# Performance work log

Hardware: AMD Instinct MI355X
Metric: run time of the kernel (lower is better)

Reference implementation:

```python
import jax, jax.numpy as jnp
import numpy as np

N, E, D, C, L = 50000, 600000, 128, 40, 4  # nodes, edges, feat dim, classes, conv layers
BN_EPS = 1e-5


def hardswish(x):
    return x * jnp.clip(x + 3.0, 0.0, 6.0) * (1.0 / 6.0)


def setup_inputs() -> dict:
    key = jax.random.key(0)
    ks = jax.random.split(key, 20)
    x = jax.random.normal(ks[0], (N, D), dtype=jnp.float32)
    src = jax.random.randint(ks[1], (E,), 0, N)
    off = jax.random.randint(ks[2], (E,), 1, N)  # guarantees dst != src
    dst = (src + off) % N
    s = 1.0 / np.sqrt(D)
    inp = {
        'x': x, 'src': src, 'dst': dst,
        # per-layer attentional aggregation params (stacked over L layers)
        'Wg': jax.random.normal(ks[3], (L, D, 1), dtype=jnp.float32) * s,
        'bg': jnp.zeros((L, 1), dtype=jnp.float32),
        'Wt': jax.random.normal(ks[4], (L, D, D), dtype=jnp.float32) * s,
        'bt': jnp.zeros((L, D), dtype=jnp.float32),
        # per-layer transform: Linear -> BN(eval) -> Hardswish -> Linear
        'W1': jax.random.normal(ks[5], (L, D, D), dtype=jnp.float32) * s,
        'b1': jnp.zeros((L, D), dtype=jnp.float32),
        'bn_gamma': 0.5 + jax.random.uniform(ks[6], (L, D), dtype=jnp.float32),
        'bn_beta': jax.random.normal(ks[7], (L, D), dtype=jnp.float32) * 0.1,
        'bn_mean': jax.random.normal(ks[8], (L, D), dtype=jnp.float32) * 0.1,
        'bn_var': 0.5 + jax.random.uniform(ks[9], (L, D), dtype=jnp.float32),
        'W2': jax.random.normal(ks[10], (L, D, D), dtype=jnp.float32) * s,
        'b2': jnp.zeros((L, D), dtype=jnp.float32),
        # post_mp head
        'Wp1': jax.random.normal(ks[11], (D, D), dtype=jnp.float32) * s,
        'bp1': jnp.zeros((D,), dtype=jnp.float32),
        'Wp2': jax.random.normal(ks[12], (D, C), dtype=jnp.float32) * s,
        'bp2': jnp.zeros((C,), dtype=jnp.float32),
    }
    return inp


def reference(x, src, dst, Wg, bg, Wt, bt, W1, b1, bn_gamma, bn_beta, bn_mean, bn_var, W2, b2, Wp1, bp1, Wp2, bp2):
    n = x.shape[0]
    loops = jnp.arange(n)
    s = jnp.concatenate([src, loops])  # add_remaining_self_loops
    d = jnp.concatenate([dst, loops])
    h = x
    for i in range(Wg.shape[0]):
        xj = h[s]                                    # gather source feats [E+N, D]
        gate = (xj @ Wg[i] + bg[i])[:, 0]            # attention logit per edge
        m = jax.ops.segment_max(gate, d, num_segments=n)
        e = jnp.exp(gate - m[d])
        denom = jax.ops.segment_sum(e, d, num_segments=n)
        w = e / denom[d]                             # per-dest softmax weight
        hj = xj @ Wt[i] + bt[i]                      # transform_node_feats
        agg = jax.ops.segment_sum(w[:, None] * hj, d, num_segments=n)
        z = agg @ W1[i] + b1[i]
        z = (z - bn_mean[i]) * jax.lax.rsqrt(bn_var[i] + BN_EPS) * bn_gamma[i] + bn_beta[i]
        z = hardswish(z)
        h = z @ W2[i] + b2[i]
        h = hardswish(h)                             # outer F.hardswish in GNN.forward
    h = hardswish(h @ Wp1 + bp1)
    logits = h @ Wp2 + bp2
    return jax.nn.log_softmax(logits, axis=-1)
```

## Files before the change

### kernel.cpp

```cpp
#include <hip/hip_runtime.h>
#include <math.h>

#define FD 128
#define CLS 40
#define BN_EPS 1e-5f
#define AS_STRIDE 136

typedef short short8 __attribute__((ext_vector_type(8)));
typedef float floatx4 __attribute__((ext_vector_type(4)));
typedef unsigned short ushort4v __attribute__((ext_vector_type(4)));
typedef unsigned short u16;
typedef unsigned int u32;

__device__ __forceinline__ u16 bf16_of(float v) {
    unsigned int u = __float_as_uint(v);
    unsigned int r = u + 0x7FFFu + ((u >> 16) & 1u);
    return (u16)(r >> 16);
}
__device__ __forceinline__ float bf16f(u16 h) {
    return __uint_as_float(((unsigned int)h) << 16);
}
__device__ __forceinline__ float blo(u32 v) { return __uint_as_float(v << 16); }
__device__ __forceinline__ float bhi(u32 v) { return __uint_as_float(v & 0xFFFF0000u); }
__device__ __forceinline__ float hswish(float x) {
    return x * fminf(fmaxf(x + 3.0f, 0.0f), 6.0f) * (1.0f / 6.0f);
}

__global__ void hist_kernel(const int* __restrict__ dst, int* __restrict__ cnt,
                            int* __restrict__ rank, int E) {
    int e = blockIdx.x * 256 + threadIdx.x;
    if (e < E) rank[e] = atomicAdd(&cnt[dst[e]], 1);
}

__global__ __launch_bounds__(256) void scan_p1(const int* __restrict__ cnt,
                                               int* __restrict__ bsum, int Nn) {
    const int t = threadIdx.x, b = blockIdx.x;
    int i = b * 256 + t;
    int v = (i < Nn) ? cnt[i] : 0;
    #pragma unroll
    for (int o = 32; o; o >>= 1) v += __shfl_xor(v, o);
    __shared__ int ws[4];
    if ((t & 63) == 0) ws[t >> 6] = v;
    __syncthreads();
    if (t == 0) bsum[b] = ws[0] + ws[1] + ws[2] + ws[3];
}

__global__ __launch_bounds__(256) void scan_p2(int* __restrict__ bsum, int NB,
                                               int* __restrict__ offs, int Nn) {
    __shared__ int wsum[4];
    __shared__ int run_s;
    const int t = threadIdx.x, lane = t & 63, wid = t >> 6;
    if (t == 0) run_s = 0;
    __syncthreads();
    for (int base = 0; base < NB; base += 256) {
        int i = base + t;
        int v = (i < NB) ? bsum[i] : 0;
        int x = v;
        #pragma unroll
        for (int o = 1; o < 64; o <<= 1) {
            int y = __shfl_up(x, o);
            if (lane >= o) x += y;
        }
        if (lane == 63) wsum[wid] = x;
        __syncthreads();
        int pre = run_s;
        #pragma unroll
        for (int w = 0; w < 4; ++w) { if (w < wid) pre += wsum[w]; }
        if (i < NB) bsum[i] = pre + x - v;
        __syncthreads();
        if (t == 0) run_s += wsum[0] + wsum[1] + wsum[2] + wsum[3];
        __syncthreads();
    }
    if (t == 0) offs[Nn] = run_s;
}

__global__ __launch_bounds__(256) void scan_p3(const int* __restrict__ cnt,
                                               const int* __restrict__ bsum,
                                               int* __restrict__ offs, int Nn) {
    __shared__ int wsum[4];
    const int t = threadIdx.x, b = blockIdx.x, lane = t & 63, wid = t >> 6;
    int i = b * 256 + t;
    int v = (i < Nn) ? cnt[i] : 0;
    int x = v;
    #pragma unroll
    for (int o = 1; o < 64; o <<= 1) {
        int y = __shfl_up(x, o);
        if (lane >= o) x += y;
    }
    if (lane == 63) wsum[wid] = x;
    __syncthreads();
    int pre = bsum[b];
    #pragma unroll
    for (int w = 0; w < 4; ++w) { if (w < wid) pre += wsum[w]; }
    if (i < Nn) offs[i] = pre + x - v;
}

__global__ void scatter_kernel(const int* __restrict__ src, const int* __restrict__ dst,
                               const int* __restrict__ offs, const int* __restrict__ rank,
                               int* __restrict__ col, int E) {
    int e = blockIdx.x * 256 + threadIdx.x;
    if (e < E) col[offs[dst[e]] + rank[e]] = src[e];
}

__global__ void prep_weights(const float* __restrict__ Wt, const float* __restrict__ W1,
                             const float* __restrict__ W2, const float* __restrict__ Wp1,
                             const float* __restrict__ Wp2, const float* __restrict__ Wg,
                             u16* __restrict__ wbuf, int L) {
    const int m = blockIdx.y;
    const int id = blockIdx.x * 256 + threadIdx.x;
    const int nsq = 3 * L + 1;
    if (m < nsq) {
        u16* base = wbuf + (size_t)m * 32768;
        const float* src = (m < L) ? Wt + m * 16384
                         : (m < 2 * L) ? W1 + (m - L) * 16384
                         : (m < 3 * L) ? W2 + (m - 2 * L) * 16384
                         : Wp1;
        int n = id >> 7, k = id & 127;
        base[n * 128 + k] = bf16_of(src[k * 128 + n]);
    } else if (m == nsq) {
        if (id >= 48 * 128) return;
        u16* base = wbuf + (size_t)m * 32768;
        int n = id >> 7, k = id & 127;
        base[n * 128 + k] = bf16_of((n < CLS) ? Wp2[k * CLS + n] : 0.f);
    } else {
        int gi = m - (nsq + 1);
        if (id >= 2048) return;
        u16* base = wbuf + (size_t)(nsq + 1) * 32768 + (size_t)gi * 4096;
        base[id] = bf16_of((id < 128) ? Wg[gi * 128 + id] : 0.f);
    }
}

__device__ __forceinline__ void stage_f32(const float* __restrict__ A, int m0, int M,
                                          u16* As, int t) {
    #pragma unroll
    for (int i = 0; i < 8; ++i) {
        int id = i * 256 + t;
        int row = id >> 5, c4 = id & 31;
        float4 v = make_float4(0.f, 0.f, 0.f, 0.f);
        if (m0 + row < M) v = ((const float4*)A)[(size_t)(m0 + row) * 32 + c4];
        ushort4v hh = {bf16_of(v.x), bf16_of(v.y), bf16_of(v.z), bf16_of(v.w)};
        *(ushort4v*)(&As[row * AS_STRIDE + c4 * 4]) = hh;
    }
}

__device__ __forceinline__ void stage_bf16(const u16* __restrict__ A, int m0, int M,
                                           u16* As, int t) {
    #pragma unroll
    for (int i = 0; i < 4; ++i) {
        int id = i * 256 + t;
        int row = id >> 4, c8 = id & 15;
        short8 v = {0, 0, 0, 0, 0, 0, 0, 0};
        if (m0 + row < M) v = ((const short8*)A)[(size_t)(m0 + row) * 16 + c8];
        *(short8*)(&As[row * AS_STRIDE + c8 * 8]) = v;
    }
}

struct Bfrags { short8 h[2][4]; };

__device__ __forceinline__ void load_B(const u16* __restrict__ Bh,
                                       int ct0, int l16, int quad, Bfrags& f) {
    #pragma unroll
    for (int c = 0; c < 2; ++c)
        #pragma unroll
        for (int kc = 0; kc < 4; ++kc) {
            int boff = ((ct0 + c) * 16 + l16) * 128 + kc * 32 + quad * 8;
            f.h[c][kc] = *(const short8*)(&Bh[boff]);
        }
}

__device__ __forceinline__ void gemm_ct2(const u16* As, const Bfrags& f, int l16, int quad,
                                         floatx4 (&acc)[4][2]) {
    #pragma unroll
    for (int kc = 0; kc < 4; ++kc) {
        short8 a[4];
        #pragma unroll
        for (int rt = 0; rt < 4; ++rt)
            a[rt] = *(const short8*)(&As[(rt * 16 + l16) * AS_STRIDE + kc * 32 + quad * 8]);
        #pragma unroll
        for (int rt = 0; rt < 4; ++rt)
            #pragma unroll
            for (int c = 0; c < 2; ++c)
                acc[rt][c] = __builtin_amdgcn_mfma_f32_16x16x32_bf16(a[rt], f.h[c][kc], acc[rt][c], 0, 0, 0);
    }
}

#define ZERO_ACC(acc) { _Pragma("unroll") for (int rt = 0; rt < 4; ++rt) \
    { acc[rt][0] = (floatx4){0.f,0.f,0.f,0.f}; acc[rt][1] = (floatx4){0.f,0.f,0.f,0.f}; } }

__device__ __forceinline__ void gate_panel(const u16* As, const u16* __restrict__ Gh,
                                           const float* __restrict__ bg,
                                           float* __restrict__ gate,
                                           int m0, int M, int l16, int quad) {
    floatx4 gacc[4];
    #pragma unroll
    for (int rt = 0; rt < 4; ++rt) gacc[rt] = (floatx4){0.f, 0.f, 0.f, 0.f};
    #pragma unroll
    for (int kc = 0; kc < 4; ++kc) {
        int boff = l16 * 128 + kc * 32 + quad * 8;
        short8 gh = *(const short8*)(&Gh[boff]);
        #pragma unroll
        for (int rt = 0; rt < 4; ++rt) {
            short8 a = *(const short8*)(&As[(rt * 16 + l16) * AS_STRIDE + kc * 32 + quad * 8]);
            gacc[rt] = __builtin_amdgcn_mfma_f32_16x16x32_bf16(a, gh, gacc[rt], 0, 0, 0);
        }
    }
    if (l16 == 0) {
        float b0 = bg[0];
        #pragma unroll
        for (int rt = 0; rt < 4; ++rt)
            #pragma unroll
            for (int reg = 0; reg < 4; ++reg) {
                int row = m0 + rt * 16 + quad * 4 + reg;
                if (row < M) gate[row] = gacc[rt][reg] + b0;
            }
    }
}

__global__ __launch_bounds__(256, 3) void gemm_gate_kernel(
    const float* __restrict__ Af,
    const u16* __restrict__ Gh, const float* __restrict__ bg,
    const u16* __restrict__ Bh, const float* __restrict__ bt,
    u16* __restrict__ ht, float* __restrict__ gate, int M) {
    __shared__ __align__(16) u16 As[64 * AS_STRIDE];
    const int t = threadIdx.x, m0 = blockIdx.x * 64;
    const int w = t >> 6, lane = t & 63, l16 = lane & 15, quad = lane >> 4, ct0 = w * 2;
    Bfrags f;
    load_B(Bh, ct0, l16, quad, f);
    stage_f32(Af, m0, M, As, t);
    __syncthreads();
    floatx4 acc[4][2];
    ZERO_ACC(acc);
    gemm_ct2(As, f, l16, quad, acc);
    if (w == 0) gate_panel(As, Gh, bg, gate, m0, M, l16, quad);
    #pragma unroll
    for (int c = 0; c < 2; ++c) {
        int cc = (ct0 + c) * 16 + l16;
        float b = bt[cc];
        #pragma unroll
        for (int rt = 0; rt < 4; ++rt)
            #pragma unroll
            for (int reg = 0; reg < 4; ++reg) {
                int row = m0 + rt * 16 + quad * 4 + reg;
                if (row < M) ht[(size_t)row * 128 + cc] = bf16_of(acc[rt][c][reg] + b);
            }
    }
}

__global__ __launch_bounds__(256) void agg_kernel(const float* __restrict__ gate,
                                                  const u32* __restrict__ ht32,
                                                  const int* __restrict__ offs,
                                                  const int* __restrict__ col,
                                                  u32* __restrict__ aggb, int Nn) {
    int gt = blockIdx.x * 256 + threadIdx.x;
    int n = gt >> 6, lane = gt & 63;
    if (n >= Nn) return;
    int beg = offs[n], end = offs[n + 1];
    float gs = gate[n];
    float denom0 = 1.0f, denom1 = 0.f;
    u32 sv = ht32[(size_t)n * 64 + lane];
    float a0 = blo(sv), a1 = bhi(sv);
    float b0 = 0.f, b1 = 0.f;
    int e = beg;
    for (; e + 8 <= end; e += 8) {
        int c[8];
        #pragma unroll
        for (int j = 0; j < 8; ++j) c[j] = col[e + j];
        float g[8];
        #pragma unroll
        for (int j = 0; j < 8; ++j) g[j] = gate[c[j]];
        u32 v[8];
        #pragma unroll
        for (int j = 0; j < 8; ++j) v[j] = ht32[(size_t)c[j] * 64 + lane];
        float wj[8];
        #pragma unroll
        for (int j = 0; j < 8; ++j) wj[j] = __expf(g[j] - gs);
        denom0 += (wj[0] + wj[1]) + (wj[2] + wj[3]);
        denom1 += (wj[4] + wj[5]) + (wj[6] + wj[7]);
        #pragma unroll
        for (int j = 0; j < 4; ++j) {
            a0 += wj[j] * blo(v[j]);
            a1 += wj[j] * bhi(v[j]);
        }
        #pragma unroll
        for (int j = 4; j < 8; ++j) {
            b0 += wj[j] * blo(v[j]);
            b1 += wj[j] * bhi(v[j]);
        }
    }
    for (; e < end; ++e) {
        int c = col[e];
        float w = __expf(gate[c] - gs);
        u32 v = ht32[(size_t)c * 64 + lane];
        denom0 += w;
        a0 += w * blo(v);
        a1 += w * bhi(v);
    }
    float inv = 1.0f / (denom0 + denom1);
    float r0 = (a0 + b0) * inv, r1 = (a1 + b1) * inv;
    aggb[(size_t)n * 64 + lane] = (u32)bf16_of(r0) | ((u32)bf16_of(r1) << 16);
}

__global__ __launch_bounds__(256, 3) void layer_mid_kernel(
    const u16* __restrict__ A,
    const u16* __restrict__ B1h, const float* __restrict__ b1,
    const float* __restrict__ bng, const float* __restrict__ bnb,
    const float* __restrict__ bnm, const float* __restrict__ bnv,
    const u16* __restrict__ B2h, const float* __restrict__ b2,
    const u16* __restrict__ Wth, const float* __restrict__ bt,
    const u16* __restrict__ Gh, const float* __restrict__ bg,
    u16* __restrict__ htb, float* __restrict__ gate, int M) {
    __shared__ __align__(16) u16 As[64 * AS_STRIDE];
    __shared__ __align__(16) u16 Zs[64 * AS_STRIDE];
    const int t = threadIdx.x, m0 = blockIdx.x * 64;
    const int w = t >> 6, lane = t & 63, l16 = lane & 15, quad = lane >> 4, ct0 = w * 2;
    Bfrags f;
    load_B(B1h, ct0, l16, quad, f);
    stage_bf16(A, m0, M, As, t);
    __syncthreads();
    floatx4 acc[4][2];
    ZERO_ACC(acc);
    gemm_ct2(As, f, l16, quad, acc);
    #pragma unroll
    for (int c = 0; c < 2; ++c) {
        int cc = (ct0 + c) * 16 + l16;
        float sc = bng[cc] * rsqrtf(bnv[cc] + BN_EPS);
        float sh = bnb[cc] - bnm[cc] * sc;
        float bb = b1[cc];
        #pragma unroll
        for (int rt = 0; rt < 4; ++rt)
            #pragma unroll
            for (int reg = 0; reg < 4; ++reg) {
                int r = rt * 16 + quad * 4 + reg;
                Zs[r * AS_STRIDE + cc] = bf16_of(hswish((acc[rt][c][reg] + bb) * sc + sh));
            }
    }
    load_B(B2h, ct0, l16, quad, f);
    __syncthreads();
    ZERO_ACC(acc);
    gemm_ct2(Zs, f, l16, quad, acc);
    #pragma unroll
    for (int c = 0; c < 2; ++c) {
        int cc = (ct0 + c) * 16 + l16;
        float b = b2[cc];
        #pragma unroll
        for (int rt = 0; rt < 4; ++rt)
            #pragma unroll
            for (int reg = 0; reg < 4; ++reg) {
                int r = rt * 16 + quad * 4 + reg;
                As[r * AS_STRIDE + cc] = bf16_of(hswish(acc[rt][c][reg] + b));
            }
    }
    load_B(Wth, ct0, l16, quad, f);
    __syncthreads();
    ZERO_ACC(acc);
    gemm_ct2(As, f, l16, quad, acc);
    if (w == 0) gate_panel(As, Gh, bg, gate, m0, M, l16, quad);
    #pragma unroll
    for (int c = 0; c < 2; ++c) {
        int cc = (ct0 + c) * 16 + l16;
        float b = bt[cc];
        #pragma unroll
        for (int rt = 0; rt < 4; ++rt)
            #pragma unroll
            for (int reg = 0; reg < 4; ++reg) {
                int row = m0 + rt * 16 + quad * 4 + reg;
                if (row < M) htb[(size_t)row * 128 + cc] = bf16_of(acc[rt][c][reg] + b);
            }
    }
}

__global__ __launch_bounds__(256, 3) void layer_final_kernel(
    const u16* __restrict__ A,
    const u16* __restrict__ B1h, const float* __restrict__ b1,
    const float* __restrict__ bng, const float* __restrict__ bnb,
    const float* __restrict__ bnm, const float* __restrict__ bnv,
    const u16* __restrict__ B2h, const float* __restrict__ b2,
    const u16* __restrict__ P1h, const float* __restrict__ bp1,
    const u16* __restrict__ P2h, const float* __restrict__ bp2,
    float* __restrict__ out, int M) {
    __shared__ __align__(16) u16 As[64 * AS_STRIDE];
    __shared__ __align__(16) u16 Zs[64 * AS_STRIDE];
    const int t = threadIdx.x, m0 = blockIdx.x * 64;
    const int w = t >> 6, lane = t & 63, l16 = lane & 15, quad = lane >> 4, ct0 = w * 2;
    Bfrags f;
    load_B(B1h, ct0, l16, quad, f);
    stage_bf16(A, m0, M, As, t);
    __syncthreads();
    floatx4 acc[4][2];
    ZERO_ACC(acc);
    gemm_ct2(As, f, l16, quad, acc);
    #pragma unroll
    for (int c = 0; c < 2; ++c) {
        int cc = (ct0 + c) * 16 + l16;
        float sc = bng[cc] * rsqrtf(bnv[cc] + BN_EPS);
        float sh = bnb[cc] - bnm[cc] * sc;
        float bb = b1[cc];
        #pragma unroll
        for (int rt = 0; rt < 4; ++rt)
            #pragma unroll
            for (int reg = 0; reg < 4; ++reg) {
                int r = rt * 16 + quad * 4 + reg;
                Zs[r * AS_STRIDE + cc] = bf16_of(hswish((acc[rt][c][reg] + bb) * sc + sh));
            }
    }
    load_B(B2h, ct0, l16, quad, f);
    __syncthreads();
    ZERO_ACC(acc);
    gemm_ct2(Zs, f, l16, quad, acc);
    #pragma unroll
    for (int c = 0; c < 2; ++c) {
        int cc = (ct0 + c) * 16 + l16;
        float b = b2[cc];
        #pragma unroll
        for (int rt = 0; rt < 4; ++rt)
            #pragma unroll
            for (int reg = 0; reg < 4; ++reg) {
                int r = rt * 16 + quad * 4 + reg;
                As[r * AS_STRIDE + cc] = bf16_of(hswish(acc[rt][c][reg] + b));
            }
    }
    load_B(P1h, ct0, l16, quad, f);
    __syncthreads();
    ZERO_ACC(acc);
    gemm_ct2(As, f, l16, quad, acc);
    #pragma unroll
    for (int c = 0; c < 2; ++c) {
        int cc = (ct0 + c) * 16 + l16;
        float bb = bp1[cc];
        #pragma unroll
        for (int rt = 0; rt < 4; ++rt)
            #pragma unroll
            for (int reg = 0; reg < 4; ++reg) {
                int r = rt * 16 + quad * 4 + reg;
                Zs[r * AS_STRIDE + cc] = bf16_of(hswish(acc[rt][c][reg] + bb));
            }
    }
    __syncthreads();
    const int wr0 = w * 16;
    floatx4 acc2[3];
    #pragma unroll
    for (int ct = 0; ct < 3; ++ct) acc2[ct] = (floatx4){0.f, 0.f, 0.f, 0.f};
    #pragma unroll
    for (int kc = 0; kc < 4; ++kc) {
        short8 a = *(const short8*)(&Zs[(wr0 + l16) * AS_STRIDE + kc * 32 + quad * 8]);
        #pragma unroll
        for (int ct = 0; ct < 3; ++ct) {
            int boff = (ct * 16 + l16) * 128 + kc * 32 + quad * 8;
            short8 bh = *(const short8*)(&P2h[boff]);
            acc2[ct] = __builtin_amdgcn_mfma_f32_16x16x32_bf16(a, bh, acc2[ct], 0, 0, 0);
        }
    }
    #pragma unroll
    for (int reg = 0; reg < 4; ++reg) {
        float v[3];
        #pragma unroll
        for (int ct = 0; ct < 3; ++ct) {
            int c = ct * 16 + l16;
            v[ct] = (c < CLS) ? acc2[ct][reg] + bp2[c] : -INFINITY;
        }
        float mx = fmaxf(fmaxf(v[0], v[1]), v[2]);
        #pragma unroll
        for (int o = 1; o < 16; o <<= 1) mx = fmaxf(mx, __shfl_xor(mx, o));
        float s = 0.f;
        #pragma unroll
        for (int ct = 0; ct < 3; ++ct) s += (v[ct] > -INFINITY) ? __expf(v[ct] - mx) : 0.f;
        #pragma unroll
        for (int o = 1; o < 16; o <<= 1) s += __shfl_xor(s, o);
        float lse = mx + __logf(s);
        int row = m0 + wr0 + quad * 4 + reg;
        if (row < M) {
            #pragma unroll
            for (int ct = 0; ct < 3; ++ct) {
                int c = ct * 16 + l16;
                if (c < CLS) out[(size_t)row * CLS + c] = v[ct] - lse;
            }
        }
    }
}

extern "C" void kernel_launch(void* const* d_in, const int* in_sizes, int n_in,
                              void* d_out, int out_size, void* d_ws, size_t ws_size,
                              hipStream_t stream) {
    const float* x   = (const float*)d_in[0];
    const int*   src = (const int*)d_in[1];
    const int*   dst = (const int*)d_in[2];
    const float* Wg  = (const float*)d_in[3];
    const float* bg  = (const float*)d_in[4];
    const float* Wt  = (const float*)d_in[5];
    const float* bt  = (const float*)d_in[6];
    const float* W1  = (const float*)d_in[7];
    const float* b1  = (const float*)d_in[8];
    const float* bng = (const float*)d_in[9];
    const float* bnb = (const float*)d_in[10];
    const float* bnm = (const float*)d_in[11];
    const float* bnv = (const float*)d_in[12];
    const float* W2  = (const float*)d_in[13];
    const float* b2  = (const float*)d_in[14];
    const float* Wp1 = (const float*)d_in[15];
    const float* bp1 = (const float*)d_in[16];
    const float* Wp2 = (const float*)d_in[17];
    const float* bp2 = (const float*)d_in[18];
    float* out = (float*)d_out;

    const int N = in_sizes[0] / FD;
    const int E = in_sizes[1];
    const int L = in_sizes[3] / FD;
    const int nsq = 3 * L + 1;
    const int NB = (N + 255) / 256;

    u16* htb    = (u16*)d_ws;
    u16* aggb   = htb + (size_t)N * FD;
    float* gate = (float*)(aggb + (size_t)N * FD);
    u16* wbuf   = (u16*)(gate + N);
    size_t wslots = (size_t)(nsq + 1) * 32768 + (size_t)L * 4096;
    int* counts = (int*)(wbuf + wslots);
    int* offs   = counts + N;
    int* rank   = offs + (N + 1);
    int* col    = rank + E;
    int* bsum   = col + E;

    hipMemsetAsync(counts, 0, N * sizeof(int), stream);
    hist_kernel<<<(E + 255) / 256, 256, 0, stream>>>(dst, counts, rank, E);
    prep_weights<<<dim3(64, nsq + 1 + L), 256, 0, stream>>>(Wt, W1, W2, Wp1, Wp2, Wg, wbuf, L);
    scan_p1<<<NB, 256, 0, stream>>>(counts, bsum, N);
    scan_p2<<<1, 256, 0, stream>>>(bsum, NB, offs, N);
    scan_p3<<<NB, 256, 0, stream>>>(counts, bsum, offs, N);
    scatter_kernel<<<(E + 255) / 256, 256, 0, stream>>>(src, dst, offs, rank, col, E);

    const int grid_g = (N + 63) / 64;
    const int wave_grid = (N + 3) / 4;

    u16* gp0 = wbuf + (size_t)(nsq + 1) * 32768;
    u16* wt0 = wbuf;
    gemm_gate_kernel<<<grid_g, 256, 0, stream>>>(x, gp0, bg, wt0, bt, htb, gate, N);
    for (int i = 0; i < L; ++i) {
        agg_kernel<<<wave_grid, 256, 0, stream>>>(gate, (const u32*)htb,
                                                  offs, col, (u32*)aggb, N);
        u16* w1 = wbuf + (size_t)(L + i) * 32768;
        u16* w2 = wbuf + (size_t)(2 * L + i) * 32768;
        if (i < L - 1) {
            u16* wtn = wbuf + (size_t)(i + 1) * 32768;
            u16* gpn = wbuf + (size_t)(nsq + 1) * 32768 + (size_t)(i + 1) * 4096;
            layer_mid_kernel<<<grid_g, 256, 0, stream>>>(aggb,
                w1, b1 + i * FD,
                bng + i * FD, bnb + i * FD, bnm + i * FD, bnv + i * FD,
                w2, b2 + i * FD,
                wtn, bt + (i + 1) * FD,
                gpn, bg + (i + 1),
                htb, gate, N);
        } else {
            u16* wp1 = wbuf + (size_t)(3 * L) * 32768;
            u16* wp2 = wbuf + (size_t)nsq * 32768;
            layer_final_kernel<<<grid_g, 256, 0, stream>>>(aggb,
                w1, b1 + i * FD,
                bng + i * FD, bnb + i * FD, bnm + i * FD, bnv + i * FD,
                w2, b2 + i * FD,
                wp1, bp1,
                wp2, bp2,
                out, N);
        }
    }
}
```

Before: 421.1 us.

## Fuse edge softmax aggregation into per-layer MLP kernels with ping-pong buffers

Removes the separate aggregation kernel and computes the softmax-weighted neighbor aggregation directly into shared memory inside the layer_mid and layer_final kernels. Each wave handles 16 destination rows serially before the GEMMs. This saves a launch per layer and the write and re-read of the aggregated bf16 buffer. Because the fused kernel reads the previous features while writing new ones, the ht and gate buffers are double-buffered. The cost is lower parallelism for the latency-bound gather, since each wave now processes 16 rows in sequence at 3 blocks per CU, and the GEMM work sits behind the gather.

```diff
diff --git a/kernel.cpp b/kernel.cpp
--- a/kernel.cpp
+++ b/kernel.cpp
@@ -143,18 +143,6 @@
     }
 }
 
-__device__ __forceinline__ void stage_bf16(const u16* __restrict__ A, int m0, int M,
-                                           u16* As, int t) {
-    #pragma unroll
-    for (int i = 0; i < 4; ++i) {
-        int id = i * 256 + t;
-        int row = id >> 4, c8 = id & 15;
-        short8 v = {0, 0, 0, 0, 0, 0, 0, 0};
-        if (m0 + row < M) v = ((const short8*)A)[(size_t)(m0 + row) * 16 + c8];
-        *(short8*)(&As[row * AS_STRIDE + c8 * 8]) = v;
-    }
-}
-
 struct Bfrags { short8 h[2][4]; };
 
 __device__ __forceinline__ void load_B(const u16* __restrict__ Bh,
@@ -213,6 +201,64 @@
                 int row = m0 + rt * 16 + quad * 4 + reg;
                 if (row < M) gate[row] = gacc[rt][reg] + b0;
             }
+    }
+}
+
+__device__ __forceinline__ void agg_rows(const float* __restrict__ gate,
+                                         const u32* __restrict__ ht32,
+                                         const int* __restrict__ offs,
+                                         const int* __restrict__ col,
+                                         u16* As, int m0, int M, int w, int lane) {
+    for (int s = 0; s < 16; ++s) {
+        int row = w * 16 + s;
+        int n = m0 + row;
+        u32 packed = 0;
+        if (n < M) {
+            int beg = offs[n], end = offs[n + 1];
+            float gs = gate[n];
+            float denom0 = 1.0f, denom1 = 0.f;
+            u32 sv = ht32[(size_t)n * 64 + lane];
+            float a0 = blo(sv), a1 = bhi(sv);
+            float b0 = 0.f, b1 = 0.f;
+            int e = beg;
+            for (; e + 8 <= end; e += 8) {
+                int c[8];
+                #pragma unroll
+                for (int j = 0; j < 8; ++j) c[j] = col[e + j];
+                float g[8];
+                #pragma unroll
+                for (int j = 0; j < 8; ++j) g[j] = gate[c[j]];
+                u32 v[8];
+                #pragma unroll
+                for (int j = 0; j < 8; ++j) v[j] = ht32[(size_t)c[j] * 64 + lane];
+                float wj[8];
+                #pragma unroll
+                for (int j = 0; j < 8; ++j) wj[j] = __expf(g[j] - gs);
+                denom0 += (wj[0] + wj[1]) + (wj[2] + wj[3]);
+                denom1 += (wj[4] + wj[5]) + (wj[6] + wj[7]);
+                #pragma unroll
+                for (int j = 0; j < 4; ++j) {
+                    a0 += wj[j] * blo(v[j]);
+                    a1 += wj[j] * bhi(v[j]);
+                }
+                #pragma unroll
+                for (int j = 4; j < 8; ++j) {
+                    b0 += wj[j] * blo(v[j]);
+                    b1 += wj[j] * bhi(v[j]);
+                }
+            }
+            for (; e < end; ++e) {
+                int c = col[e];
+                float wj = __expf(gate[c] - gs);
+                u32 v = ht32[(size_t)c * 64 + lane];
+                denom0 += wj;
+                a0 += wj * blo(v);
+                a1 += wj * bhi(v);
+            }
+            float inv = 1.0f / (denom0 + denom1);
+            packed = (u32)bf16_of((a0 + b0) * inv) | ((u32)bf16_of((a1 + b1) * inv) << 16);
+        }
+        *(u32*)(&As[row * AS_STRIDE + lane * 2]) = packed;
     }
 }
 
@@ -246,76 +292,23 @@
     }
 }
 
-__global__ __launch_bounds__(256) void agg_kernel(const float* __restrict__ gate,
-                                                  const u32* __restrict__ ht32,
-                                                  const int* __restrict__ offs,
-                                                  const int* __restrict__ col,
-                                                  u32* __restrict__ aggb, int Nn) {
-    int gt = blockIdx.x * 256 + threadIdx.x;
-    int n = gt >> 6, lane = gt & 63;
-    if (n >= Nn) return;
-    int beg = offs[n], end = offs[n + 1];
-    float gs = gate[n];
-    float denom0 = 1.0f, denom1 = 0.f;
-    u32 sv = ht32[(size_t)n * 64 + lane];
-    float a0 = blo(sv), a1 = bhi(sv);
-    float b0 = 0.f, b1 = 0.f;
-    int e = beg;
-    for (; e + 8 <= end; e += 8) {
-        int c[8];
-        #pragma unroll
-        for (int j = 0; j < 8; ++j) c[j] = col[e + j];
-        float g[8];
-        #pragma unroll
-        for (int j = 0; j < 8; ++j) g[j] = gate[c[j]];
-        u32 v[8];
-        #pragma unroll
-        for (int j = 0; j < 8; ++j) v[j] = ht32[(size_t)c[j] * 64 + lane];
-        float wj[8];
-        #pragma unroll
-        for (int j = 0; j < 8; ++j) wj[j] = __expf(g[j] - gs);
-        denom0 += (wj[0] + wj[1]) + (wj[2] + wj[3]);
-        denom1 += (wj[4] + wj[5]) + (wj[6] + wj[7]);
-        #pragma unroll
-        for (int j = 0; j < 4; ++j) {
-            a0 += wj[j] * blo(v[j]);
-            a1 += wj[j] * bhi(v[j]);
-        }
-        #pragma unroll
-        for (int j = 4; j < 8; ++j) {
-            b0 += wj[j] * blo(v[j]);
-            b1 += wj[j] * bhi(v[j]);
-        }
-    }
-    for (; e < end; ++e) {
-        int c = col[e];
-        float w = __expf(gate[c] - gs);
-        u32 v = ht32[(size_t)c * 64 + lane];
-        denom0 += w;
-        a0 += w * blo(v);
-        a1 += w * bhi(v);
-    }
-    float inv = 1.0f / (denom0 + denom1);
-    float r0 = (a0 + b0) * inv, r1 = (a1 + b1) * inv;
-    aggb[(size_t)n * 64 + lane] = (u32)bf16_of(r0) | ((u32)bf16_of(r1) << 16);
-}
-
 __global__ __launch_bounds__(256, 3) void layer_mid_kernel(
-    const u16* __restrict__ A,
+    const float* __restrict__ gate_in, const u32* __restrict__ ht_in,
+    const int* __restrict__ offs, const int* __restrict__ col,
     const u16* __restrict__ B1h, const float* __restrict__ b1,
     const float* __restrict__ bng, const float* __restrict__ bnb,
     const float* __restrict__ bnm, const float* __restrict__ bnv,
     const u16* __restrict__ B2h, const float* __restrict__ b2,
     const u16* __restrict__ Wth, const float* __restrict__ bt,
     const u16* __restrict__ Gh, const float* __restrict__ bg,
-    u16* __restrict__ htb, float* __restrict__ gate, int M) {
+    u16* __restrict__ ht_out, float* __restrict__ gate_out, int M) {
     __shared__ __align__(16) u16 As[64 * AS_STRIDE];
     __shared__ __align__(16) u16 Zs[64 * AS_STRIDE];
     const int t = threadIdx.x, m0 = blockIdx.x * 64;
     const int w = t >> 6, lane = t & 63, l16 = lane & 15, quad = lane >> 4, ct0 = w * 2;
+    agg_rows(gate_in, ht_in, offs, col, As, m0, M, w, lane);
     Bfrags f;
     load_B(B1h, ct0, l16, quad, f);
-    stage_bf16(A, m0, M, As, t);
     __syncthreads();
     floatx4 acc[4][2];
     ZERO_ACC(acc);
@@ -354,7 +347,7 @@
     __syncthreads();
     ZERO_ACC(acc);
     gemm_ct2(As, f, l16, quad, acc);
-    if (w == 0) gate_panel(As, Gh, bg, gate, m0, M, l16, quad);
+    if (w == 0) gate_panel(As, Gh, bg, gate_out, m0, M, l16, quad);
     #pragma unroll
     for (int c = 0; c < 2; ++c) {
         int cc = (ct0 + c) * 16 + l16;
@@ -364,13 +357,14 @@
             #pragma unroll
             for (int reg = 0; reg < 4; ++reg) {
                 int row = m0 + rt * 16 + quad * 4 + reg;
-                if (row < M) htb[(size_t)row * 128 + cc] = bf16_of(acc[rt][c][reg] + b);
+                if (row < M) ht_out[(size_t)row * 128 + cc] = bf16_of(acc[rt][c][reg] + b);
             }
     }
 }
 
 __global__ __launch_bounds__(256, 3) void layer_final_kernel(
-    const u16* __restrict__ A,
+    const float* __restrict__ gate_in, const u32* __restrict__ ht_in,
+    const int* __restrict__ offs, const int* __restrict__ col,
     const u16* __restrict__ B1h, const float* __restrict__ b1,
     const float* __restrict__ bng, const float* __restrict__ bnb,
     const float* __restrict__ bnm, const float* __restrict__ bnv,
@@ -382,9 +376,9 @@
     __shared__ __align__(16) u16 Zs[64 * AS_STRIDE];
     const int t = threadIdx.x, m0 = blockIdx.x * 64;
     const int w = t >> 6, lane = t & 63, l16 = lane & 15, quad = lane >> 4, ct0 = w * 2;
+    agg_rows(gate_in, ht_in, offs, col, As, m0, M, w, lane);
     Bfrags f;
     load_B(B1h, ct0, l16, quad, f);
-    stage_bf16(A, m0, M, As, t);
     __syncthreads();
     floatx4 acc[4][2];
     ZERO_ACC(acc);
@@ -508,10 +502,11 @@
     const int nsq = 3 * L + 1;
     const int NB = (N + 255) / 256;
 
-    u16* htb    = (u16*)d_ws;
-    u16* aggb   = htb + (size_t)N * FD;
-    float* gate = (float*)(aggb + (size_t)N * FD);
-    u16* wbuf   = (u16*)(gate + N);
+    u16* ht0    = (u16*)d_ws;
+    u16* ht1    = ht0 + (size_t)N * FD;
+    float* ga0  = (float*)(ht1 + (size_t)N * FD);
+    float* ga1  = ga0 + N;
+    u16* wbuf   = (u16*)(ga1 + N);
     size_t wslots = (size_t)(nsq + 1) * 32768 + (size_t)L * 4096;
     int* counts = (int*)(wbuf + wslots);
     int* offs   = counts + N;
@@ -528,30 +523,33 @@
     scatter_kernel<<<(E + 255) / 256, 256, 0, stream>>>(src, dst, offs, rank, col, E);
 
     const int grid_g = (N + 63) / 64;
-    const int wave_grid = (N + 3) / 4;
 
     u16* gp0 = wbuf + (size_t)(nsq + 1) * 32768;
     u16* wt0 = wbuf;
-    gemm_gate_kernel<<<grid_g, 256, 0, stream>>>(x, gp0, bg, wt0, bt, htb, gate, N);
+    gemm_gate_kernel<<<grid_g, 256, 0, stream>>>(x, gp0, bg, wt0, bt, ht0, ga0, N);
+    u16* ht_in = ht0; float* ga_in = ga0;
+    u16* ht_nx = ht1; float* ga_nx = ga1;
     for (int i = 0; i < L; ++i) {
-        agg_kernel<<<wave_grid, 256, 0, stream>>>(gate, (const u32*)htb,
-                                                  offs, col, (u32*)aggb, N);
         u16* w1 = wbuf + (size_t)(L + i) * 32768;
         u16* w2 = wbuf + (size_t)(2 * L + i) * 32768;
         if (i < L - 1) {
             u16* wtn = wbuf + (size_t)(i + 1) * 32768;
             u16* gpn = wbuf + (size_t)(nsq + 1) * 32768 + (size_t)(i + 1) * 4096;
-            layer_mid_kernel<<<grid_g, 256, 0, stream>>>(aggb,
+            layer_mid_kernel<<<grid_g, 256, 0, stream>>>(
+                ga_in, (const u32*)ht_in, offs, col,
                 w1, b1 + i * FD,
                 bng + i * FD, bnb + i * FD, bnm + i * FD, bnv + i * FD,
                 w2, b2 + i * FD,
                 wtn, bt + (i + 1) * FD,
                 gpn, bg + (i + 1),
-                htb, gate, N);
+                ht_nx, ga_nx, N);
+            u16* tb = ht_in; ht_in = ht_nx; ht_nx = tb;
+            float* tg = ga_in; ga_in = ga_nx; ga_nx = tg;
         } else {
             u16* wp1 = wbuf + (size_t)(3 * L) * 32768;
             u16* wp2 = wbuf + (size_t)nsq * 32768;
-            layer_final_kernel<<<grid_g, 256, 0, stream>>>(aggb,
+            layer_final_kernel<<<grid_g, 256, 0, stream>>>(
+                ga_in, (const u32*)ht_in, offs, col,
                 w1, b1 + i * FD,
                 bng + i * FD, bnb + i * FD, bnm + i * FD, bnv + i * FD,
                 w2, b2 + i * FD,
```

Measured after the change: 476.4 us. 1.13x slower.
